# Kernel optimization log

Measured on AMD Instinct MI355X. Metric: run time of the kernel, lower is better.

The kernel has to match this reference:

```python
import jax, jax.numpy as jnp
import numpy as np

B = 16384
ED = 32          # embed_dim
NF = 16          # num_filters
KS = [1, 3, 5, 7, 9]
LENS = {"pep": 12, "a1": 7, "a2": 8, "a3": 22, "b1": 6, "b2": 7, "b3": 23}


def setup_inputs() -> dict:
    key = jax.random.key(0)
    keys = jax.random.split(key, 32)
    ki = iter(keys)
    inp = {}
    for name, L in LENS.items():
        inp[name] = jax.random.normal(next(ki), (B, ED, L), dtype=jnp.float32)
    # conv weights: one stack of 7 convs per kernel size; w{k}: [7, NF, ED, k], bias c{k}: [7, NF]
    for k in KS:
        fan_in = ED * k
        bound = 1.0 / np.sqrt(fan_in)
        inp[f"w{k}"] = jax.random.uniform(next(ki), (7, NF, ED, k), jnp.float32, -bound, bound)
        inp[f"c{k}"] = jax.random.uniform(next(ki), (7, NF), jnp.float32, -bound, bound)
    dbound = 1.0 / np.sqrt(NF * 35)
    inp["dw"] = jax.random.uniform(next(ki), (NF * 35, 1), jnp.float32, -dbound, dbound)
    inp["db"] = jax.random.uniform(next(ki), (1,), jnp.float32, -dbound, dbound)
    return inp


def _branch(x, w, b):
    # x: [B, ED, L], w: [NF, ED, k], b: [NF] -> [B, NF] (conv 'same' + relu + global max)
    y = jax.lax.conv_general_dilated(x, w, window_strides=(1,), padding="SAME",
                                     dimension_numbers=("NCH", "OIH", "NCH"))
    y = jax.nn.relu(y + b[None, :, None])
    return jnp.max(y, axis=2)


def reference(pep, a1, a2, a3, b1, b2, b3, w1, w3, w5, w7, w9, c1, c3, c5, c7, c9, dw, db):
    xs = [pep, a1, a2, a3, b1, b2, b3]
    ws = {1: w1, 3: w3, 5: w5, 7: w7, 9: w9}
    cs = {1: c1, 3: c3, 5: c5, 7: c7, 9: c9}
    feats = []
    for i, x in enumerate(xs):  # fixed 7 inputs
        for k in KS:            # fixed 5 kernel sizes
            feats.append(_branch(x, ws[k][i], cs[k][i]))
    feat = jnp.concatenate(feats, axis=1)        # [B, 35*NF]
    out = jax.nn.sigmoid(feat @ dw + db)         # [B, 1]
    return jnp.squeeze(out, axis=-1)             # [B]
```

## Files before the change

### kernel.cpp

```cpp
#include <hip/hip_runtime.h>
#include <cmath>

namespace {

using bf16x8 = __attribute__((ext_vector_type(8))) short;
using f32x4  = __attribute__((ext_vector_type(4))) float;

constexpr int NT = 192;
constexpr int NS = 16;
constexpr int TILE_BYTES = NS * 31 * 32 * 2;
constexpr int B = 16384;

__device__ __forceinline__ short f2bf(float f) {
  unsigned u = __float_as_uint(f);
  return (short)((u + 0x7FFFu + ((u >> 16) & 1u)) >> 16);
}

__device__ __forceinline__ int gidx(int s, int q, int cq) {
  return (s * 31 + q) * 4 + ((cq ^ ((s >> 1) + (q >> 1))) & 3);
}

__device__ __forceinline__ bf16x8 ldcol(const char* smem, int s, int cq, int q) {
  return *(const bf16x8*)(smem + (gidx(s, q, cq) << 4));
}

template<int K1, int K2>
__device__ __forceinline__ void run_role(
    const char* __restrict__ smem, int s, int cq, int f,
    const float* __restrict__ wk1, const float* __restrict__ ck1,
    const float* __restrict__ wk2, const float* __restrict__ ck2,
    const float* __restrict__ dw, int i, int L, f32x4& dvec)
{
  constexpr int KK1 = (K1 - 1) / 2;
  constexpr int KK2 = (K2 > 0) ? (K2 - 1) / 2 : 0;

  bf16x8 wf1[K1];
  #pragma unroll
  for (int t = 0; t < K1; ++t) {
    const float* wp = wk1 + (size_t)((i * 16 + f) * 32 + cq * 8) * K1 + t;
    bf16x8 v;
    #pragma unroll
    for (int j = 0; j < 8; ++j) v[j] = f2bf(wp[(size_t)j * K1]);
    wf1[t] = v;
  }
  bf16x8 wf2[(K2 > 0) ? K2 : 1];
  if constexpr (K2 > 0) {
    #pragma unroll
    for (int t = 0; t < K2; ++t) {
      const float* wp = wk2 + (size_t)((i * 16 + f) * 32 + cq * 8) * K2 + t;
      bf16x8 v;
      #pragma unroll
      for (int j = 0; j < 8; ++j) v[j] = f2bf(wp[(size_t)j * K2]);
      wf2[t] = v;
    }
  }

  const float b1 = ck1[i * 16 + f];
  float b2 = 0.f;
  if constexpr (K2 > 0) b2 = ck2[i * 16 + f];

  f32x4 mx1 = {0.f, 0.f, 0.f, 0.f};
  f32x4 mx2 = {0.f, 0.f, 0.f, 0.f};

  bf16x8 af[K1];
  #pragma unroll
  for (int j = 0; j < K1; ++j) af[j] = ldcol(smem, s, cq, 4 - KK1 + j);

  auto body = [&](int p, int pi) {
    f32x4 aa = {b1, b1, b1, b1};
    f32x4 ab = {0.f, 0.f, 0.f, 0.f};
    #pragma unroll
    for (int t = 0; t < K1; ++t) {
      if (t & 1)
        ab = __builtin_amdgcn_mfma_f32_16x16x32_bf16(af[(pi + t) % K1], wf1[t], ab, 0, 0, 0);
      else
        aa = __builtin_amdgcn_mfma_f32_16x16x32_bf16(af[(pi + t) % K1], wf1[t], aa, 0, 0, 0);
    }
    if constexpr (K2 > 0) {
      f32x4 ac = {b2, b2, b2, b2};
      #pragma unroll
      for (int t = 0; t < K2; ++t)
        ac = __builtin_amdgcn_mfma_f32_16x16x32_bf16(af[(pi + (KK1 - KK2) + t) % K1], wf2[t], ac, 0, 0, 0);
      #pragma unroll
      for (int r = 0; r < 4; ++r) mx2[r] = fmaxf(mx2[r], ac[r]);
    }
    #pragma unroll
    for (int r = 0; r < 4; ++r) mx1[r] = fmaxf(mx1[r], aa[r] + ab[r]);
    if (p + pi + 1 < L)
      af[pi] = ldcol(smem, s, cq, p + pi + 5 + KK1);
  };

  int p = 0;
  for (; p + K1 <= L; p += K1) {
    #pragma unroll
    for (int pi = 0; pi < K1; ++pi) body(p, pi);
  }
  #pragma unroll
  for (int pi = 0; pi < K1 - 1; ++pi)
    if (p + pi < L) body(p, pi);

  {
    const float dv1 = dw[(i * 5 + KK1) * 16 + f];
    #pragma unroll
    for (int r = 0; r < 4; ++r) dvec[r] = fmaf(mx1[r], dv1, dvec[r]);
  }
  if constexpr (K2 > 0) {
    const float dv2 = dw[(i * 5 + KK2) * 16 + f];
    #pragma unroll
    for (int r = 0; r < 4; ++r) dvec[r] = fmaf(mx2[r], dv2, dvec[r]);
  }
}

__global__ __launch_bounds__(NT, 2) void nettcr_mfma(
    const float* __restrict__ x0, const float* __restrict__ x1,
    const float* __restrict__ x2, const float* __restrict__ x3,
    const float* __restrict__ x4, const float* __restrict__ x5,
    const float* __restrict__ x6,
    const float* __restrict__ w1, const float* __restrict__ c1,
    const float* __restrict__ w3, const float* __restrict__ c3,
    const float* __restrict__ w5, const float* __restrict__ c5,
    const float* __restrict__ w7, const float* __restrict__ c7,
    const float* __restrict__ w9, const float* __restrict__ c9,
    const float* __restrict__ dw,
    float* __restrict__ part)
{
  __shared__ __align__(16) char smem[TILE_BYTES];
  const int tid  = threadIdx.x;
  const int lane = tid & 63;
  const int wid  = tid >> 6;
  const int h    = blockIdx.x & 1;
  const int b0   = (blockIdx.x >> 1) * NS;
  const int s    = lane & 15;
  const int cq   = lane >> 4;
  const int f    = lane & 15;

  f32x4 dvec = {0.f, 0.f, 0.f, 0.f};

  const int nin = h ? 4 : 3;
  for (int j = 0; j < nin; ++j) {
    const float* xi; int i, L;
    if (h == 0) {
      switch (j) {
        case 0:  i = 0; xi = x0; L = 12; break;
        case 1:  i = 3; xi = x3; L = 22; break;
        default: i = 5; xi = x5; L = 7;  break;
      }
    } else {
      switch (j) {
        case 0:  i = 1; xi = x1; L = 7;  break;
        case 1:  i = 2; xi = x2; L = 8;  break;
        case 2:  i = 4; xi = x4; L = 6;  break;
        default: i = 6; xi = x6; L = 23; break;
      }
    }
    __syncthreads();
    for (int e = tid; e < 64 * L; e += NT) {
      const int l  = e % L;
      const int rr = e / L;
      const int cg = rr & 3;
      const int ss = rr >> 2;
      const float* src = xi + ((size_t)(b0 + ss) * 32 + cg * 8) * L + l;
      bf16x8 pk;
      #pragma unroll
      for (int jj = 0; jj < 8; ++jj) pk[jj] = f2bf(src[(size_t)jj * L]);
      *(bf16x8*)(smem + (gidx(ss, l + 4, cg) << 4)) = pk;
    }
    for (int e = tid; e < 512; e += NT) {
      const int q8 = e & 7;
      const int q  = (q8 < 4) ? q8 : (L + q8);
      const int cg = (e >> 3) & 3;
      const int ss = e >> 5;
      bf16x8 z = {0, 0, 0, 0, 0, 0, 0, 0};
      *(bf16x8*)(smem + (gidx(ss, q, cg) << 4)) = z;
    }
    __syncthreads();

    if (wid == 0)
      run_role<9, 0>(smem, s, cq, f, w9, c9, nullptr, nullptr, dw, i, L, dvec);
    else if (wid == 1)
      run_role<7, 1>(smem, s, cq, f, w7, c7, w1, c1, dw, i, L, dvec);
    else
      run_role<5, 3>(smem, s, cq, f, w5, c5, w3, c3, dw, i, L, dvec);
  }

  __syncthreads();
  float* red = (float*)smem;
  *(f32x4*)&red[(wid * 64 + lane) * 4] = dvec;
  __syncthreads();
  if (tid < 16) {
    float sum = 0.f;
    const int g4 = tid >> 2, r = tid & 3;
    for (int w = 0; w < 3; ++w)
      #pragma unroll
      for (int f2 = 0; f2 < 16; ++f2)
        sum += red[(w * 64 + g4 * 16 + f2) * 4 + r];
    part[h * B + b0 + tid] = sum;
  }
}

__global__ void combine_sigmoid(const float* __restrict__ part,
                                const float* __restrict__ db,
                                float* __restrict__ out)
{
  const int i = blockIdx.x * blockDim.x + threadIdx.x;
  if (i < B) {
    const float sum = part[i] + part[B + i] + db[0];
    out[i] = 1.0f / (1.0f + expf(-sum));
  }
}

}

extern "C" void kernel_launch(void* const* d_in, const int* in_sizes, int n_in,
                              void* d_out, int out_size, void* d_ws, size_t ws_size,
                              hipStream_t stream) {
  (void)ws_size; (void)out_size;
  const float* xs[7];
  for (int i = 0; i < 7; ++i) xs[i] = (const float*)d_in[i];

  const float* wptr[5] = {nullptr, nullptr, nullptr, nullptr, nullptr};
  const float* cptr[5] = {nullptr, nullptr, nullptr, nullptr, nullptr};
  const float* dw = nullptr;
  const float* db = nullptr;
  int c_seen = 0;
  for (int idx = 7; idx < n_in; ++idx) {
    const int sz = in_sizes[idx];
    const float* p = (const float*)d_in[idx];
    if (sz == 1) { db = p; }
    else if (sz == 16 * 35) { dw = p; }
    else if (sz == 7 * 16) { cptr[c_seen++] = p; }
    else {
      const int k = sz / (7 * 16 * 32);
      wptr[(k - 1) / 2] = p;
    }
  }

  float* part = (float*)d_ws;

  dim3 grid(2 * (B / NS)), block(NT);
  hipLaunchKernelGGL(nettcr_mfma, grid, block, 0, stream,
                     xs[0], xs[1], xs[2], xs[3], xs[4], xs[5], xs[6],
                     wptr[0], cptr[0], wptr[1], cptr[1], wptr[2], cptr[2],
                     wptr[3], cptr[3], wptr[4], cptr[4], dw, part);

  hipLaunchKernelGGL(combine_sigmoid, dim3((B + 255) / 256), dim3(256), 0, stream,
                     part, db, (float*)d_out);
}
```

Before: 118.8 us.

## Split work into one block per input sequence and raise MFMA wave priority

Each block now handles a single input sequence for a 16-sample tile, so the grid grows from 2×1024 to 7×1024 blocks. This removes the per-input loop and its inner barriers. The combine kernel now sums seven partial buffers instead of two. s_setprio is also raised around the MFMA loop so compute waves are favoured over waves that are loading. The trade-off is more block launch overhead, per-block weight reloads, more workspace traffic and uneven block lengths (L from 6 to 23).

```diff
diff --git a/kernel.cpp b/kernel.cpp
--- a/kernel.cpp
+++ b/kernel.cpp
@@ -10,6 +10,7 @@
 constexpr int NS = 16;
 constexpr int TILE_BYTES = NS * 31 * 32 * 2;
 constexpr int B = 16384;
+constexpr int NTILE = B / NS;
 
 __device__ __forceinline__ short f2bf(float f) {
   unsigned u = __float_as_uint(f);
@@ -90,6 +91,7 @@
       af[pi] = ldcol(smem, s, cq, p + pi + 5 + KK1);
   };
 
+  __builtin_amdgcn_s_setprio(1);
   int p = 0;
   for (; p + K1 <= L; p += K1) {
     #pragma unroll
@@ -98,6 +100,7 @@
   #pragma unroll
   for (int pi = 0; pi < K1 - 1; ++pi)
     if (p + pi < L) body(p, pi);
+  __builtin_amdgcn_s_setprio(0);
 
   {
     const float dv1 = dw[(i * 5 + KK1) * 16 + f];
@@ -128,60 +131,52 @@
   const int tid  = threadIdx.x;
   const int lane = tid & 63;
   const int wid  = tid >> 6;
-  const int h    = blockIdx.x & 1;
-  const int b0   = (blockIdx.x >> 1) * NS;
+  const int bx   = blockIdx.x;
+  const int i    = bx % 7;
+  const int b0   = (bx / 7) * NS;
   const int s    = lane & 15;
   const int cq   = lane >> 4;
   const int f    = lane & 15;
 
+  const float* xi; int L;
+  switch (i) {
+    case 0: xi = x0; L = 12; break;
+    case 1: xi = x1; L = 7;  break;
+    case 2: xi = x2; L = 8;  break;
+    case 3: xi = x3; L = 22; break;
+    case 4: xi = x4; L = 6;  break;
+    case 5: xi = x5; L = 7;  break;
+    default: xi = x6; L = 23; break;
+  }
+
+  for (int e = tid; e < 64 * L; e += NT) {
+    const int l  = e % L;
+    const int rr = e / L;
+    const int cg = rr & 3;
+    const int ss = rr >> 2;
+    const float* src = xi + ((size_t)(b0 + ss) * 32 + cg * 8) * L + l;
+    bf16x8 pk;
+    #pragma unroll
+    for (int jj = 0; jj < 8; ++jj) pk[jj] = f2bf(src[(size_t)jj * L]);
+    *(bf16x8*)(smem + (gidx(ss, l + 4, cg) << 4)) = pk;
+  }
+  for (int e = tid; e < 512; e += NT) {
+    const int q8 = e & 7;
+    const int q  = (q8 < 4) ? q8 : (L + q8);
+    const int cg = (e >> 3) & 3;
+    const int ss = e >> 5;
+    bf16x8 z = {0, 0, 0, 0, 0, 0, 0, 0};
+    *(bf16x8*)(smem + (gidx(ss, q, cg) << 4)) = z;
+  }
+  __syncthreads();
+
   f32x4 dvec = {0.f, 0.f, 0.f, 0.f};
-
-  const int nin = h ? 4 : 3;
-  for (int j = 0; j < nin; ++j) {
-    const float* xi; int i, L;
-    if (h == 0) {
-      switch (j) {
-        case 0:  i = 0; xi = x0; L = 12; break;
-        case 1:  i = 3; xi = x3; L = 22; break;
-        default: i = 5; xi = x5; L = 7;  break;
-      }
-    } else {
-      switch (j) {
-        case 0:  i = 1; xi = x1; L = 7;  break;
-        case 1:  i = 2; xi = x2; L = 8;  break;
-        case 2:  i = 4; xi = x4; L = 6;  break;
-        default: i = 6; xi = x6; L = 23; break;
-      }
-    }
-    __syncthreads();
-    for (int e = tid; e < 64 * L; e += NT) {
-      const int l  = e % L;
-      const int rr = e / L;
-      const int cg = rr & 3;
-      const int ss = rr >> 2;
-      const float* src = xi + ((size_t)(b0 + ss) * 32 + cg * 8) * L + l;
-      bf16x8 pk;
-      #pragma unroll
-      for (int jj = 0; jj < 8; ++jj) pk[jj] = f2bf(src[(size_t)jj * L]);
-      *(bf16x8*)(smem + (gidx(ss, l + 4, cg) << 4)) = pk;
-    }
-    for (int e = tid; e < 512; e += NT) {
-      const int q8 = e & 7;
-      const int q  = (q8 < 4) ? q8 : (L + q8);
-      const int cg = (e >> 3) & 3;
-      const int ss = e >> 5;
-      bf16x8 z = {0, 0, 0, 0, 0, 0, 0, 0};
-      *(bf16x8*)(smem + (gidx(ss, q, cg) << 4)) = z;
-    }
-    __syncthreads();
-
-    if (wid == 0)
-      run_role<9, 0>(smem, s, cq, f, w9, c9, nullptr, nullptr, dw, i, L, dvec);
-    else if (wid == 1)
-      run_role<7, 1>(smem, s, cq, f, w7, c7, w1, c1, dw, i, L, dvec);
-    else
-      run_role<5, 3>(smem, s, cq, f, w5, c5, w3, c3, dw, i, L, dvec);
-  }
+  if (wid == 0)
+    run_role<9, 0>(smem, s, cq, f, w9, c9, nullptr, nullptr, dw, i, L, dvec);
+  else if (wid == 1)
+    run_role<7, 1>(smem, s, cq, f, w7, c7, w1, c1, dw, i, L, dvec);
+  else
+    run_role<5, 3>(smem, s, cq, f, w5, c5, w3, c3, dw, i, L, dvec);
 
   __syncthreads();
   float* red = (float*)smem;
@@ -194,7 +189,7 @@
       #pragma unroll
       for (int f2 = 0; f2 < 16; ++f2)
         sum += red[(w * 64 + g4 * 16 + f2) * 4 + r];
-    part[h * B + b0 + tid] = sum;
+    part[i * B + b0 + tid] = sum;
   }
 }
 
@@ -204,7 +199,9 @@
 {
   const int i = blockIdx.x * blockDim.x + threadIdx.x;
   if (i < B) {
-    const float sum = part[i] + part[B + i] + db[0];
+    float sum = db[0];
+    #pragma unroll
+    for (int j = 0; j < 7; ++j) sum += part[j * B + i];
     out[i] = 1.0f / (1.0f + expf(-sum));
   }
 }
@@ -237,7 +234,7 @@
 
   float* part = (float*)d_ws;
 
-  dim3 grid(2 * (B / NS)), block(NT);
+  dim3 grid(7 * NTILE), block(NT);
   hipLaunchKernelGGL(nettcr_mfma, grid, block, 0, stream,
                      xs[0], xs[1], xs[2], xs[3], xs[4], xs[5], xs[6],
                      wptr[0], cptr[0], wptr[1], cptr[1], wptr[2], cptr[2],
```

After: 113.2 us. 1.05x faster.
